# Performance work log

Measured on AMD Instinct MI355X. Metric: run time of the kernel, lower is better.

Reference implementation:

```python
import jax, jax.numpy as jnp
import numpy as np

TOP_K = 2


def setup_inputs() -> dict:
    key = jax.random.key(0)
    ks = jax.random.split(key, 6)
    B, S, D, E = 4, 2048, 1024, 8
    d_ff = 4 * D
    x = jax.random.normal(ks[0], (B, S, D), dtype=jnp.float32)
    router_w = jax.random.normal(ks[1], (E, D), dtype=jnp.float32) * 0.02
    w_fc = jax.random.normal(ks[2], (E, d_ff, D), dtype=jnp.float32) * 0.02
    w_proj = jax.random.normal(ks[3], (E, D, d_ff), dtype=jnp.float32) * 0.02
    shared_fc = jax.random.normal(ks[4], (d_ff, D), dtype=jnp.float32) * 0.02
    shared_proj = jax.random.normal(ks[5], (D, d_ff), dtype=jnp.float32) * 0.02
    return {"x": x, "router_w": router_w, "w_fc": w_fc, "w_proj": w_proj,
            "shared_fc": shared_fc, "shared_proj": shared_proj}


def _mlp(x, w_fc, w_proj):
    # c_proj(relu(c_fc(x))^2); torch Linear: y = x @ W.T
    return jnp.square(jax.nn.relu(x @ w_fc.T)) @ w_proj.T


def reference(x, router_w, w_fc, w_proj, shared_fc, shared_proj):
    B, S, D = x.shape
    E = router_w.shape[0]
    T = B * S
    flat = x.reshape(T, D)
    # Router: softmax in fp32, top-k, renormalize
    logits = flat @ router_w.T                                   # [T, E]
    probs = jax.nn.softmax(logits.astype(jnp.float32), axis=-1)
    topk_p, topk_i = jax.lax.top_k(probs, TOP_K)                 # [T, k]
    topk_w = (topk_p / jnp.maximum(topk_p.sum(-1, keepdims=True), 1e-9)).astype(flat.dtype)
    # Dense combine weights [T, E]: scatter normalized top-k weights per token
    combine = jnp.zeros((T, E), dtype=flat.dtype)
    combine = combine.at[jnp.arange(T)[:, None], topk_i].add(topk_w)
    # Expert compute (loop over small fixed E), weighted combine
    out = jnp.zeros_like(flat)
    for e in range(E):
        out = out + _mlp(flat, w_fc[e], w_proj[e]) * combine[:, e:e + 1]
    # Shared expert applied to all tokens
    out = out + _mlp(flat, shared_fc, shared_proj)
    return out.reshape(B, S, D)
```

## Files before the change

kernel.cpp:

```cpp
#include <hip/hip_runtime.h>

#define DEVFN __device__ __forceinline__

typedef _Float16 f16x8 __attribute__((ext_vector_type(8)));
typedef float f32x4 __attribute__((ext_vector_type(4)));

static constexpr int T   = 8192;
static constexpr int D   = 1024;
static constexpr int E   = 8;
static constexpr int DFF = 4096;
static constexpr int NG  = E + 1;
static constexpr int RTOT = 3*T;
static constexpr int MAXRT = (2*T)/256 + E + T/256;

DEVFN unsigned short f2h_bits(float v){
  _Float16 h = (_Float16)v;
  return __builtin_bit_cast(unsigned short, h);
}

DEVFN void gload_lds16(const void* g, void* l){
  __builtin_amdgcn_global_load_lds((const __attribute__((address_space(1))) void*)g,
                                   (__attribute__((address_space(3))) void*)l, 16, 0, 0);
}

__global__ __launch_bounds__(256) void cast_all_kernel(
    const float* __restrict__ s0, const float* __restrict__ s1,
    const float* __restrict__ s2, const float* __restrict__ s3,
    unsigned short* __restrict__ d0, unsigned short* __restrict__ d1,
    unsigned short* __restrict__ d2, unsigned short* __restrict__ d3,
    int n0, int n1, int n2, int n3){
  int total = n0 + n1 + n2 + n3;
  for (int j = blockIdx.x*256 + threadIdx.x; j < total; j += gridDim.x*256){
    const float* sp; unsigned short* dp; int loc = j;
    if (loc < n0){ sp = s0; dp = d0; }
    else if ((loc -= n0) < n1){ sp = s1; dp = d1; }
    else if ((loc -= n1) < n2){ sp = s2; dp = d2; }
    else { loc -= n2; sp = s3; dp = d3; }
    float4 v = ((const float4*)sp)[loc];
    ushort4 o;
    o.x = f2h_bits(v.x); o.y = f2h_bits(v.y); o.z = f2h_bits(v.z); o.w = f2h_bits(v.w);
    ((ushort4*)dp)[loc] = o;
  }
}

__global__ __launch_bounds__(256) void router_kernel(const float* __restrict__ x,
    const float* __restrict__ rw, unsigned short* __restrict__ xb,
    int* __restrict__ tok_e, float* __restrict__ tok_w, int* __restrict__ counts){
  const int lane = threadIdx.x & 63;
  const int t = blockIdx.x*4 + (threadIdx.x >> 6);
  const float4* xp = (const float4*)(x + (size_t)t*D);
  ushort4* xo = (ushort4*)(xb + (size_t)t*D);
  float acc[E];
#pragma unroll
  for (int e=0;e<E;e++) acc[e]=0.f;
#pragma unroll
  for (int i=0;i<4;i++){
    float4 xv = xp[lane + (i<<6)];
    ushort4 o; o.x=f2h_bits(xv.x); o.y=f2h_bits(xv.y); o.z=f2h_bits(xv.z); o.w=f2h_bits(xv.w);
    xo[lane + (i<<6)] = o;
#pragma unroll
    for (int e=0;e<E;e++){
      float4 wv = ((const float4*)(rw + e*D))[lane + (i<<6)];
      acc[e] = fmaf(xv.x,wv.x, fmaf(xv.y,wv.y, fmaf(xv.z,wv.z, fmaf(xv.w,wv.w, acc[e]))));
    }
  }
#pragma unroll
  for (int e=0;e<E;e++){
#pragma unroll
    for (int off=32; off>0; off>>=1) acc[e] += __shfl_xor(acc[e], off);
  }
  if (lane==0){
    float l0=-1e30f, l1=-1e30f; int e0=0, e1=0;
#pragma unroll
    for (int e=0;e<E;e++){
      float v = acc[e];
      if (v > l0){ l1=l0; e1=e0; l0=v; e0=e; }
      else if (v > l1){ l1=v; e1=e; }
    }
    float r   = expf(l1 - l0);
    float inv = 1.f/(1.f + r);
    tok_e[2*t]   = e0; tok_e[2*t+1] = e1;
    tok_w[2*t]   = inv; tok_w[2*t+1] = r*inv;
    atomicAdd(&counts[e0], 1);
    atomicAdd(&counts[e1], 1);
  }
}

__global__ void scan_kernel(const int* __restrict__ counts, int* __restrict__ offs,
                            int* __restrict__ tile_g, int* __restrict__ tile_r0,
                            int* __restrict__ nrt){
  if (blockIdx.x==0 && threadIdx.x==0){
    int off=0, nt=0;
    for (int e=0;e<E;e++){
      offs[e]=off;
      int c = counts[e];
      int tiles = (c+255)>>8;
      for (int i=0;i<tiles;i++){ tile_g[nt]=e; tile_r0[nt]=off + (i<<8); nt++; }
      off += c;
    }
    offs[E] = off;
    for (int i=0;i<T/256;i++){ tile_g[nt]=E; tile_r0[nt]=2*T + (i<<8); nt++; }
    offs[E+1] = 3*T;
    *nrt = nt;
  }
}

__global__ __launch_bounds__(256) void scatter_kernel(const int* __restrict__ tok_e,
    const float* __restrict__ tok_w, const int* __restrict__ offs,
    int* __restrict__ fill, int* __restrict__ row_tok, float* __restrict__ row_w,
    int* __restrict__ inv2){
  int idx = blockIdx.x*256 + threadIdx.x;
  if (idx < 2*T){
    int e = tok_e[idx];
    int pos = offs[e] + atomicAdd(&fill[e], 1);
    row_tok[pos] = idx >> 1;
    row_w[pos]   = tok_w[idx];
    inv2[idx]    = pos;
  } else {
    row_tok[idx] = idx - 2*T;
    row_w[idx]   = 1.0f;
  }
}

template<int MODE>
__global__ __launch_bounds__(512, 2) void gemm8p_kernel(
    const unsigned short* __restrict__ A, const unsigned short* __restrict__ Ball,
    unsigned short* __restrict__ O,
    const int K, const int N, const int CT,
    const int* __restrict__ tile_g, const int* __restrict__ tile_r0,
    const int* __restrict__ offs, const int* __restrict__ nrt,
    const int* __restrict__ row_tok)
{
  const int nwg  = gridDim.x * gridDim.y;
  const int orig = blockIdx.y * gridDim.x + blockIdx.x;
  const int q8 = nwg >> 3, r8 = nwg & 7;
  const int xcd = orig & 7, pos = orig >> 3;
  const int wg = (xcd < r8 ? xcd*(q8+1) : r8*(q8+1) + (xcd-r8)*q8) + pos;
  const int rt = wg / CT, ct = wg - rt*CT;
  if (rt >= *nrt) return;

  const int g    = tile_g[rt];
  const int row0 = tile_r0[rt];
  const int row_end = offs[g+1];
  const unsigned short* Bp = Ball + (size_t)g * (size_t)N * (size_t)K;

  __shared__ __align__(16) unsigned short As[2*2*8192];
  __shared__ __align__(16) unsigned short Bs[2*2*8192];

  const int tid  = threadIdx.x;
  const int lane = tid & 63;
  const int wave = tid >> 6;

  const unsigned short* aS[2];
  const unsigned short* bS[2];
  int ldst[2];
#pragma unroll
  for (int c=0;c<2;c++){
    int s  = (c<<9) + tid;
    int rr = s >> 2;
    int qg = (s & 3) ^ ((rr >> 1) & 3);
    int ar = (MODE==0) ? row_tok[row0 + rr] : (row0 + rr);
    aS[c] = A  + (size_t)ar*K + qg*8;
    bS[c] = Bp + (size_t)((ct<<8) + rr)*K + qg*8;
    ldst[c] = ((c<<9) + (wave<<6))*8;
  }

#define STAGE_A(KT,KS) { _Pragma("unroll") for (int c=0;c<2;c++) \
    gload_lds16(aS[c] + (KT)*64 + (KS)*32, As + ((((KT)&1)*2+(KS))<<13) + ldst[c]); }
#define STAGE_B(KT,KS) { _Pragma("unroll") for (int c=0;c<2;c++) \
    gload_lds16(bS[c] + (KT)*64 + (KS)*32, Bs + ((((KT)&1)*2+(KS))<<13) + ldst[c]); }

  const int wm = wave >> 2, wn = wave & 3;
  const int q16g = lane >> 4;
  int aoff[8], boff[4];
#pragma unroll
  for (int m=0;m<8;m++){
    int r = (wm<<7) + (m<<4) + (lane&15);
    aoff[m] = (r<<5) + ((q16g ^ ((r>>1)&3))<<3);
  }
#pragma unroll
  for (int n=0;n<4;n++){
    int r = (wn<<6) + (n<<4) + (lane&15);
    boff[n] = (r<<5) + ((q16g ^ ((r>>1)&3))<<3);
  }

#define BARS { __builtin_amdgcn_s_barrier(); __builtin_amdgcn_sched_barrier(0); }
#define VMW(NN) asm volatile("s_waitcnt vmcnt(" #NN ")" ::: "memory");
#define DSA_LO(BUF,KS) { const unsigned short* hb = As + (((BUF)*2+(KS))<<13); \
    _Pragma("unroll") for (int m=0;m<4;m++) af[m] = *(const f16x8*)(hb + aoff[m]); }
#define DSA_HI(BUF,KS) { const unsigned short* hb = As + (((BUF)*2+(KS))<<13); \
    _Pragma("unroll") for (int m=0;m<4;m++) ag[m] = *(const f16x8*)(hb + aoff[4+m]); }
#define DSB_(BUF,KS) { const unsigned short* hb = Bs + (((BUF)*2+(KS))<<13); \
    _Pragma("unroll") for (int n=0;n<4;n++) bf[n] = *(const f16x8*)(hb + boff[n]); }
#define MFMA16(AR,SRC) { __builtin_amdgcn_s_setprio(1); \
    _Pragma("unroll") for (int m=0;m<4;m++) \
    _Pragma("unroll") for (int n=0;n<4;n++) \
      acc[(AR)*4+m][n] = __builtin_amdgcn_mfma_f32_16x16x32_f16(SRC[m], bf[n], acc[(AR)*4+m][n], 0, 0, 0); \
    __builtin_amdgcn_s_setprio(0); }

  f32x4 acc[8][4] = {};
  const int nkt = K >> 6;

  STAGE_A(0,0); STAGE_B(0,0); STAGE_A(0,1); STAGE_B(0,1);

  f16x8 af[4], ag[4], bf[4];
  for (int t=0; t<nkt; ++t){
    const int b = t & 1;
    const bool more = (t+1 < nkt);
    VMW(4); BARS;
    DSA_LO(b,0); DSB_(b,0);
    if (more) STAGE_A(t+1,0);
    MFMA16(0, af);
    BARS;
    DSA_HI(b,0);
    if (more) STAGE_B(t+1,0);
    MFMA16(1, ag);
    if (more) { VMW(4); } else { VMW(0); }
    BARS;
    DSA_LO(b,1); DSB_(b,1);
    if (more) STAGE_A(t+1,1);
    MFMA16(0, af);
    BARS;
    DSA_HI(b,1);
    if (more) STAGE_B(t+1,1);
    MFMA16(1, ag);
  }

  const int lcol = lane & 15;
  const int lrow = (lane >> 4) << 2;
#pragma unroll
  for (int m=0;m<8;m++){
#pragma unroll
    for (int q=0;q<4;q++){
      const int grow = row0 + (wm<<7) + (m<<4) + lrow + q;
      if (grow >= row_end) continue;
#pragma unroll
      for (int n=0;n<4;n++){
        const int col = (ct<<8) + (wn<<6) + (n<<4) + lcol;
        float v = acc[m][n][q];
        if constexpr (MODE==0) v = (v > 0.f) ? v*v : 0.f;
        O[(size_t)grow*N + col] = f2h_bits(v);
      }
    }
  }
#undef STAGE_A
#undef STAGE_B
#undef BARS
#undef VMW
#undef DSA_LO
#undef DSA_HI
#undef DSB_
#undef MFMA16
}

__global__ __launch_bounds__(256) void combine_kernel(const unsigned short* __restrict__ y,
    const int* __restrict__ inv2, const float* __restrict__ row_w, float* __restrict__ out){
  int gid = blockIdx.x*256 + threadIdx.x;
  int t = gid >> 7, c = gid & 127;
  int p0 = inv2[2*t], p1 = inv2[2*t+1];
  float w0 = row_w[p0], w1 = row_w[p1];
  f16x8 v0 = *(const f16x8*)(y + (size_t)p0*D      + c*8);
  f16x8 v1 = *(const f16x8*)(y + (size_t)p1*D      + c*8);
  f16x8 v2 = *(const f16x8*)(y + (size_t)(2*T+t)*D + c*8);
  float4 o0, o1;
  float r[8];
#pragma unroll
  for (int j=0;j<8;j++)
    r[j] = fmaf(w0, (float)v0[j], fmaf(w1, (float)v1[j], (float)v2[j]));
  o0.x=r[0]; o0.y=r[1]; o0.z=r[2]; o0.w=r[3];
  o1.x=r[4]; o1.y=r[5]; o1.z=r[6]; o1.w=r[7];
  float4* op = (float4*)(out + (size_t)t*D + c*8);
  op[0] = o0; op[1] = o1;
}

extern "C" void kernel_launch(void* const* d_in, const int* in_sizes, int n_in,
                              void* d_out, int out_size, void* d_ws, size_t ws_size,
                              hipStream_t stream){
  const float* x     = (const float*)d_in[0];
  const float* rw    = (const float*)d_in[1];
  const float* wfc   = (const float*)d_in[2];
  const float* wproj = (const float*)d_in[3];
  const float* sfc   = (const float*)d_in[4];
  const float* sproj = (const float*)d_in[5];
  float* out = (float*)d_out;

  char* ws = (char*)d_ws;
  size_t off = 0;
  auto alloc = [&](size_t bytes)->void*{
    void* p = ws + off; off += (bytes + 255) & ~(size_t)255; return p;
  };
  unsigned short* xb    = (unsigned short*)alloc((size_t)T*D*2);
  unsigned short* wall  = (unsigned short*)alloc((size_t)NG*DFF*D*2);
  unsigned short* wpall = (unsigned short*)alloc((size_t)NG*D*DFF*2);
  unsigned short* h     = (unsigned short*)alloc((size_t)RTOT*DFF*2);
  int*   tok_e   = (int*)  alloc((size_t)T*2*4);
  float* tok_w   = (float*)alloc((size_t)T*2*4);
  int*   row_tok = (int*)  alloc((size_t)RTOT*4);
  float* row_w   = (float*)alloc((size_t)RTOT*4);
  int*   inv2    = (int*)  alloc((size_t)2*T*4);
  int* counts  = (int*)alloc(E*4);
  int* fill    = (int*)alloc(E*4);
  int* offs    = (int*)alloc((E+2)*4);
  int* nrt     = (int*)alloc(4);
  int* tile_g  = (int*)alloc(MAXRT*4);
  int* tile_r0 = (int*)alloc(MAXRT*4);
  if (off > ws_size) return;

  unsigned short* y = wall;

  hipMemsetAsync(counts, 0, E*4, stream);
  hipMemsetAsync(fill,   0, E*4, stream);

  cast_all_kernel<<<2048, 256, 0, stream>>>(
      wfc, sfc, wproj, sproj,
      wall, wall + (size_t)E*DFF*D, wpall, wpall + (size_t)E*D*DFF,
      E*DFF*D/4, DFF*D/4, E*D*DFF/4, D*DFF/4);

  router_kernel <<<T/4, 256, 0, stream>>>(x, rw, xb, tok_e, tok_w, counts);
  scan_kernel   <<<1,   64,  0, stream>>>(counts, offs, tile_g, tile_r0, nrt);
  scatter_kernel<<<RTOT/256, 256, 0, stream>>>(tok_e, tok_w, offs, fill, row_tok, row_w, inv2);

  gemm8p_kernel<0><<<dim3(DFF/256, MAXRT), 512, 0, stream>>>(
      xb, wall, h, D, DFF, DFF/256, tile_g, tile_r0, offs, nrt, row_tok);
  gemm8p_kernel<1><<<dim3(D/256, MAXRT), 512, 0, stream>>>(
      h, wpall, y, DFF, D, D/256, tile_g, tile_r0, offs, nrt, row_tok);
  combine_kernel<<<(T*128)/256, 256, 0, stream>>>(y, inv2, row_w, out);
}
```

Measured before the change: 846.2 us.

## Restructure grouped GEMM main loop to prefetch whole k-tile with fewer barriers

The grouped expert GEMM's k-loop is rescheduled. Each k-step now issues all global-to-LDS loads for the next tile at once, loads the A and B fragments for a half-tile up front, and uses explicit lgkmcnt waits so the second batch of LDS reads overlaps the first MFMA group. This cuts the workgroup barriers per k-tile from four to two and lengthens the distance between a prefetch and its use, aiming to reduce stall time. The kernel body is also moved into a device function behind two thin wrapper kernels. The tighter manual waitcnt and sched_barrier placement may constrain the compiler's scheduling or raise register pressure at two waves per SIMD.

```diff
diff --git a/kernel.cpp b/kernel.cpp
--- a/kernel.cpp
+++ b/kernel.cpp
@@ -123,7 +123,7 @@
 }
 
 template<int MODE>
-__global__ __launch_bounds__(512, 2) void gemm8p_kernel(
+DEVFN void gemm_body(
     const unsigned short* __restrict__ A, const unsigned short* __restrict__ Ball,
     unsigned short* __restrict__ O,
     const int K, const int N, const int CT,
@@ -165,10 +165,15 @@
     ldst[c] = ((c<<9) + (wave<<6))*8;
   }
 
-#define STAGE_A(KT,KS) { _Pragma("unroll") for (int c=0;c<2;c++) \
-    gload_lds16(aS[c] + (KT)*64 + (KS)*32, As + ((((KT)&1)*2+(KS))<<13) + ldst[c]); }
-#define STAGE_B(KT,KS) { _Pragma("unroll") for (int c=0;c<2;c++) \
-    gload_lds16(bS[c] + (KT)*64 + (KS)*32, Bs + ((((KT)&1)*2+(KS))<<13) + ldst[c]); }
+#define STAGE8(KT) { \
+    _Pragma("unroll") for (int c=0;c<2;c++) \
+      gload_lds16(aS[c] + (KT)*64 +  0, As + ((((KT)&1)*2+0)<<13) + ldst[c]); \
+    _Pragma("unroll") for (int c=0;c<2;c++) \
+      gload_lds16(bS[c] + (KT)*64 +  0, Bs + ((((KT)&1)*2+0)<<13) + ldst[c]); \
+    _Pragma("unroll") for (int c=0;c<2;c++) \
+      gload_lds16(aS[c] + (KT)*64 + 32, As + ((((KT)&1)*2+1)<<13) + ldst[c]); \
+    _Pragma("unroll") for (int c=0;c<2;c++) \
+      gload_lds16(bS[c] + (KT)*64 + 32, Bs + ((((KT)&1)*2+1)<<13) + ldst[c]); }
 
   const int wm = wave >> 2, wn = wave & 3;
   const int q16g = lane >> 4;
@@ -184,46 +189,62 @@
     boff[n] = (r<<5) + ((q16g ^ ((r>>1)&3))<<3);
   }
 
-#define BARS { __builtin_amdgcn_s_barrier(); __builtin_amdgcn_sched_barrier(0); }
-#define VMW(NN) asm volatile("s_waitcnt vmcnt(" #NN ")" ::: "memory");
-#define DSA_LO(BUF,KS) { const unsigned short* hb = As + (((BUF)*2+(KS))<<13); \
-    _Pragma("unroll") for (int m=0;m<4;m++) af[m] = *(const f16x8*)(hb + aoff[m]); }
-#define DSA_HI(BUF,KS) { const unsigned short* hb = As + (((BUF)*2+(KS))<<13); \
-    _Pragma("unroll") for (int m=0;m<4;m++) ag[m] = *(const f16x8*)(hb + aoff[4+m]); }
-#define DSB_(BUF,KS) { const unsigned short* hb = Bs + (((BUF)*2+(KS))<<13); \
-    _Pragma("unroll") for (int n=0;n<4;n++) bf[n] = *(const f16x8*)(hb + boff[n]); }
-#define MFMA16(AR,SRC) { __builtin_amdgcn_s_setprio(1); \
+#define SB0 __builtin_amdgcn_sched_barrier(0);
+#define BAR __builtin_amdgcn_s_barrier();
+#define LGKM(NN) asm volatile("s_waitcnt lgkmcnt(" #NN ")" ::: "memory");
+#define VMW(NN)  asm volatile("s_waitcnt vmcnt(" #NN ")" ::: "memory");
+#define MFMA16(AR,SRC) { \
     _Pragma("unroll") for (int m=0;m<4;m++) \
     _Pragma("unroll") for (int n=0;n<4;n++) \
-      acc[(AR)*4+m][n] = __builtin_amdgcn_mfma_f32_16x16x32_f16(SRC[m], bf[n], acc[(AR)*4+m][n], 0, 0, 0); \
-    __builtin_amdgcn_s_setprio(0); }
+      acc[(AR)*4+m][n] = __builtin_amdgcn_mfma_f32_16x16x32_f16(SRC[m], bf[n], acc[(AR)*4+m][n], 0, 0, 0); }
 
   f32x4 acc[8][4] = {};
   const int nkt = K >> 6;
 
-  STAGE_A(0,0); STAGE_B(0,0); STAGE_A(0,1); STAGE_B(0,1);
+  STAGE8(0);
+  VMW(0); BAR; SB0;
 
   f16x8 af[4], ag[4], bf[4];
   for (int t=0; t<nkt; ++t){
     const int b = t & 1;
     const bool more = (t+1 < nkt);
-    VMW(4); BARS;
-    DSA_LO(b,0); DSB_(b,0);
-    if (more) STAGE_A(t+1,0);
-    MFMA16(0, af);
-    BARS;
-    DSA_HI(b,0);
-    if (more) STAGE_B(t+1,0);
-    MFMA16(1, ag);
-    if (more) { VMW(4); } else { VMW(0); }
-    BARS;
-    DSA_LO(b,1); DSB_(b,1);
-    if (more) STAGE_A(t+1,1);
-    MFMA16(0, af);
-    BARS;
-    DSA_HI(b,1);
-    if (more) STAGE_B(t+1,1);
-    MFMA16(1, ag);
+    {
+      const unsigned short* ha = As + ((b*2+0)<<13);
+      const unsigned short* hb = Bs + ((b*2+0)<<13);
+#pragma unroll
+      for (int m=0;m<4;m++) af[m] = *(const f16x8*)(ha + aoff[m]);
+#pragma unroll
+      for (int n=0;n<4;n++) bf[n] = *(const f16x8*)(hb + boff[n]);
+#pragma unroll
+      for (int m=0;m<4;m++) ag[m] = *(const f16x8*)(ha + aoff[4+m]);
+      if (more) STAGE8(t+1);
+      SB0; LGKM(4); SB0;
+      __builtin_amdgcn_s_setprio(1);
+      MFMA16(0, af);
+      SB0; LGKM(0); SB0;
+      MFMA16(1, ag);
+      __builtin_amdgcn_s_setprio(0);
+      VMW(4);
+      SB0; BAR;
+    }
+    {
+      const unsigned short* ha = As + ((b*2+1)<<13);
+      const unsigned short* hb = Bs + ((b*2+1)<<13);
+#pragma unroll
+      for (int m=0;m<4;m++) af[m] = *(const f16x8*)(ha + aoff[m]);
+#pragma unroll
+      for (int n=0;n<4;n++) bf[n] = *(const f16x8*)(hb + boff[n]);
+#pragma unroll
+      for (int m=0;m<4;m++) ag[m] = *(const f16x8*)(ha + aoff[4+m]);
+      SB0; LGKM(4); SB0;
+      __builtin_amdgcn_s_setprio(1);
+      MFMA16(0, af);
+      SB0; LGKM(0); SB0;
+      MFMA16(1, ag);
+      __builtin_amdgcn_s_setprio(0);
+      if (more) { VMW(0); }
+      SB0; BAR;
+    }
   }
 
   const int lcol = lane & 15;
@@ -243,14 +264,29 @@
       }
     }
   }
-#undef STAGE_A
-#undef STAGE_B
-#undef BARS
+#undef STAGE8
+#undef SB0
+#undef BAR
+#undef LGKM
 #undef VMW
-#undef DSA_LO
-#undef DSA_HI
-#undef DSB_
 #undef MFMA16
+}
+
+__global__ __launch_bounds__(512, 2) void gemm_fc(
+    const unsigned short* __restrict__ A, const unsigned short* __restrict__ Ball,
+    unsigned short* __restrict__ O, const int K, const int N, const int CT,
+    const int* __restrict__ tile_g, const int* __restrict__ tile_r0,
+    const int* __restrict__ offs, const int* __restrict__ nrt,
+    const int* __restrict__ row_tok){
+  gemm_body<0>(A, Ball, O, K, N, CT, tile_g, tile_r0, offs, nrt, row_tok);
+}
+__global__ __launch_bounds__(512, 2) void gemm_proj(
+    const unsigned short* __restrict__ A, const unsigned short* __restrict__ Ball,
+    unsigned short* __restrict__ O, const int K, const int N, const int CT,
+    const int* __restrict__ tile_g, const int* __restrict__ tile_r0,
+    const int* __restrict__ offs, const int* __restrict__ nrt,
+    const int* __restrict__ row_tok){
+  gemm_body<1>(A, Ball, O, K, N, CT, tile_g, tile_r0, offs, nrt, row_tok);
 }
 
 __global__ __launch_bounds__(256) void combine_kernel(const unsigned short* __restrict__ y,
@@ -320,9 +356,9 @@
   scan_kernel   <<<1,   64,  0, stream>>>(counts, offs, tile_g, tile_r0, nrt);
   scatter_kernel<<<RTOT/256, 256, 0, stream>>>(tok_e, tok_w, offs, fill, row_tok, row_w, inv2);
 
-  gemm8p_kernel<0><<<dim3(DFF/256, MAXRT), 512, 0, stream>>>(
+  gemm_fc  <<<dim3(DFF/256, MAXRT), 512, 0, stream>>>(
       xb, wall, h, D, DFF, DFF/256, tile_g, tile_r0, offs, nrt, row_tok);
-  gemm8p_kernel<1><<<dim3(D/256, MAXRT), 512, 0, stream>>>(
+  gemm_proj<<<dim3(D/256, MAXRT), 512, 0, stream>>>(
       h, wpall, y, DFF, D, D/256, tile_g, tile_r0, offs, nrt, row_tok);
   combine_kernel<<<(T*128)/256, 256, 0, stream>>>(y, inv2, row_w, out);
 }
```

New measurement: 942.7 us. 11.4% more time.
